# Optimization experiments

Measured on AMD Instinct MI355X. Metric: run time of the kernel, lower is better.

## Reference

```python
import jax, jax.numpy as jnp
import numpy as np

H = 8          # num_attention_heads
E = 768        # hidden_size
D = E // H     # attention_head_size = 96
LN_EPS = 1e-5


def setup_inputs() -> dict:
    key = jax.random.key(0)
    ks = jax.random.split(key, 12)
    B, S = 2, 2048
    inp = {
        "hidden_states": jax.random.normal(ks[0], (B, S, E), jnp.float32),
        "distance_matrix": jax.random.uniform(ks[1], (B, S, S), jnp.float32),
        "angle_matrix": jax.random.uniform(ks[2], (B, S, S), jnp.float32),
        "attention_mask": jnp.ones((B, S), jnp.float32),
        # Linear params, stored [in, out] so y = x @ W + b
        "Wq": jax.random.normal(ks[3], (E, E), jnp.float32) * 0.02,
        "bq": jnp.zeros((E,), jnp.float32),
        "Wk": jax.random.normal(ks[4], (E, E), jnp.float32) * 0.02,
        "bk": jnp.zeros((E,), jnp.float32),
        "Wv": jax.random.normal(ks[5], (E, E), jnp.float32) * 0.02,
        "bv": jnp.zeros((E,), jnp.float32),
        # distance_embedding / angle_embedding: Linear(1,1) -> scalar w,b
        "dist_w": jax.random.normal(ks[6], (), jnp.float32) * 0.5,
        "dist_b": jnp.zeros((), jnp.float32),
        "ang_w": jax.random.normal(ks[7], (), jnp.float32) * 0.5,
        "ang_b": jnp.zeros((), jnp.float32),
        "Wo": jax.random.normal(ks[8], (E, E), jnp.float32) * 0.02,
        "bo": jnp.zeros((E,), jnp.float32),
        "ln_gamma": jnp.ones((E,), jnp.float32),
        "ln_beta": jnp.zeros((E,), jnp.float32),
    }
    return inp


def _attention(hidden_states, distance_matrix, angle_matrix, attention_mask,
               Wq, bq, Wk, bk, Wv, bv, dist_w, dist_b, ang_w, ang_b,
               Wo, bo, ln_gamma, ln_beta):
    B, S, _ = hidden_states.shape
    # project and split heads -> [B, H, S, D]
    def heads(x):
        return x.reshape(B, S, H, D).transpose(0, 2, 1, 3)
    q = heads(hidden_states @ Wq + bq)
    k = heads(hidden_states @ Wk + bk)
    v = heads(hidden_states @ Wv + bv)

    scores = jnp.einsum("bhqd,bhkd->bhqk", q, k) / jnp.sqrt(jnp.float32(D))
    # fused pairwise biases, broadcast over heads
    bias = (dist_w * distance_matrix + dist_b) + (ang_w * angle_matrix + ang_b)
    scores = scores + bias[:, None, :, :]
    # additive mask: mask is [B, S] over key dim
    scores = scores + ((1.0 - attention_mask) * -10000.0)[:, None, None, :]

    probs = jax.nn.softmax(scores, axis=-1)  # dropout is identity at eval
    ctx = jnp.einsum("bhqk,bhkd->bhqd", probs, v)
    ctx = ctx.transpose(0, 2, 1, 3).reshape(B, S, E)

    out = ctx @ Wo + bo  # output dropout identity at eval
    res = out + hidden_states
    mu = jnp.mean(res, axis=-1, keepdims=True)
    var = jnp.var(res, axis=-1, keepdims=True)
    out = (res - mu) * jax.lax.rsqrt(var + LN_EPS) * ln_gamma + ln_beta
    return out, probs


def reference(hidden_states, distance_matrix, angle_matrix, attention_mask,
              Wq, bq, Wk, bk, Wv, bv, dist_w, dist_b, ang_w, ang_b,
              Wo, bo, ln_gamma, ln_beta):
    return _attention(hidden_states, distance_matrix, angle_matrix, attention_mask,
                      Wq, bq, Wk, bk, Wv, bv, dist_w, dist_b, ang_w, ang_b,
                      Wo, bo, ln_gamma, ln_beta)
```

## Files before the change

kernel.cpp:

```cpp
#include <hip/hip_runtime.h>
#include <math.h>

#define S_LEN 2048
#define BATCH 2
#define EMB 768
#define NH 8
#define HD 96
#define NTOK (BATCH*S_LEN)
#define RSQRT_D 0.10206207261596575f

typedef unsigned short u16;
typedef __attribute__((ext_vector_type(8))) short bf16x8;
typedef __attribute__((ext_vector_type(4))) float f32x4;

#define MFMA16(a,b,c) __builtin_amdgcn_mfma_f32_16x16x32_bf16(a,b,c,0,0,0)

__device__ __forceinline__ u16 f2bf(float f){
    unsigned u = __float_as_uint(f);
    return (u16)((u + 0x7fffu + ((u>>16)&1u)) >> 16);
}
__device__ __forceinline__ float bf2f(unsigned u){
    return __uint_as_float(u << 16);
}

union U16x8 { u16 u[8]; float4 f4; };
union U16x4 { u16 u[4]; uint2 v2; };

__global__ __launch_bounds__(256) void cvt_bf16_kernel(
    const float* __restrict__ src, u16* __restrict__ dst, int n4)
{
    int i = blockIdx.x * 256 + threadIdx.x;
    if (i < n4) {
        float4 v = ((const float4*)src)[i];
        U16x4 o;
        o.u[0] = f2bf(v.x); o.u[1] = f2bf(v.y); o.u[2] = f2bf(v.z); o.u[3] = f2bf(v.w);
        *(uint2*)(dst + (size_t)i*4) = o.v2;
    }
}

__global__ __launch_bounds__(256) void transcvt_kernel(
    const float* __restrict__ W, u16* __restrict__ Wt)
{
    __shared__ float T[64][65];
    const int t = threadIdx.x;
    const int k0 = blockIdx.y * 64, n0 = blockIdx.x * 64;
    #pragma unroll
    for (int i = 0; i < 4; ++i) {
        int idx = t + 256*i;
        int r = idx >> 4, c4 = idx & 15;
        float4 v = *(const float4*)(W + (size_t)(k0 + r)*EMB + n0 + c4*4);
        T[r][c4*4+0] = v.x; T[r][c4*4+1] = v.y; T[r][c4*4+2] = v.z; T[r][c4*4+3] = v.w;
    }
    __syncthreads();
    #pragma unroll
    for (int i = 0; i < 2; ++i) {
        int idx = t + 256*i;
        int n = idx >> 3, c = idx & 7;
        U16x8 o;
        #pragma unroll
        for (int e = 0; e < 8; ++e) o.u[e] = f2bf(T[c*8+e][n]);
        *(float4*)(Wt + (size_t)(n0 + n)*EMB + k0 + c*8) = o.f4;
    }
}

__global__ __launch_bounds__(256) void qkv_mfma_kernel(
    const u16* __restrict__ hsb,
    const u16* __restrict__ WqT, const float* __restrict__ bq,
    const u16* __restrict__ WkT, const float* __restrict__ bk,
    const u16* __restrict__ WvT, const float* __restrict__ bv,
    u16* __restrict__ qo, u16* __restrict__ ko, u16* __restrict__ vo)
{
    const u16* Wt; const float* bias; u16* out;
    if (blockIdx.z == 0)      { Wt = WqT; bias = bq; out = qo; }
    else if (blockIdx.z == 1) { Wt = WkT; bias = bk; out = ko; }
    else                      { Wt = WvT; bias = bv; out = vo; }

    __shared__ __align__(16) u16 As[64*64];
    __shared__ __align__(16) u16 Bs[64*64];
    const int tid = threadIdx.x;
    const int w = tid >> 6, lane = tid & 63, lh = lane & 15, g = lane >> 4;
    const int wm = w >> 1, wn = w & 1;
    const int row0 = blockIdx.y * 64, col0 = blockIdx.x * 64;

    f32x4 acc[2][2];
    #pragma unroll
    for (int i = 0; i < 2; ++i)
        #pragma unroll
        for (int j = 0; j < 2; ++j) acc[i][j] = (f32x4){0.f,0.f,0.f,0.f};

    for (int k0 = 0; k0 < EMB; k0 += 64) {
        __syncthreads();
        #pragma unroll
        for (int i = 0; i < 2; ++i) {
            int idx = tid + 256*i;
            int r = idx >> 3, c = idx & 7;
            float4 a4 = *(const float4*)(hsb + (size_t)(row0 + r)*EMB + k0 + c*8);
            *(float4*)(As + ((size_t)r*8 + (c ^ (r & 7)))*8) = a4;
            float4 b4 = *(const float4*)(Wt + (size_t)(col0 + r)*EMB + k0 + c*8);
            *(float4*)(Bs + ((size_t)r*8 + (c ^ (r & 7)))*8) = b4;
        }
        __syncthreads();
        bf16x8 af[2][2], bfr[2][2];
        #pragma unroll
        for (int mt = 0; mt < 2; ++mt)
            #pragma unroll
            for (int kk = 0; kk < 2; ++kk) {
                int r = wm*32 + mt*16 + lh;
                af[mt][kk] = *(const bf16x8*)(As + ((size_t)r*8 + ((kk*4+g) ^ (lh & 7)))*8);
            }
        #pragma unroll
        for (int nt = 0; nt < 2; ++nt)
            #pragma unroll
            for (int kk = 0; kk < 2; ++kk) {
                int r = wn*32 + nt*16 + lh;
                bfr[nt][kk] = *(const bf16x8*)(Bs + ((size_t)r*8 + ((kk*4+g) ^ (lh & 7)))*8);
            }
        #pragma unroll
        for (int mt = 0; mt < 2; ++mt)
            #pragma unroll
            for (int nt = 0; nt < 2; ++nt)
                #pragma unroll
                for (int kk = 0; kk < 2; ++kk)
                    acc[mt][nt] = MFMA16(af[mt][kk], bfr[nt][kk], acc[mt][nt]);
    }

    #pragma unroll
    for (int mt = 0; mt < 2; ++mt)
        #pragma unroll
        for (int nt = 0; nt < 2; ++nt)
            #pragma unroll
            for (int r = 0; r < 4; ++r) {
                int tt = row0 + wm*32 + mt*16 + g*4 + r;
                int o  = col0 + wn*32 + nt*16 + lh;
                float val = acc[mt][nt][r] + bias[o];
                int b = tt >> 11, s = tt & (S_LEN - 1);
                int h = o / HD, d = o - h*HD;
                out[((size_t)(b*NH + h)*S_LEN + s)*HD + d] = f2bf(val);
            }
}

__global__ __launch_bounds__(256) void vtrans_kernel(
    const u16* __restrict__ vb, u16* __restrict__ vt)
{
    const int bh = blockIdx.y;
    const int s0 = blockIdx.x * 64;
    __shared__ __align__(16) u16 T[64*96];
    const int t = threadIdx.x;
    #pragma unroll
    for (int i = 0; i < 3; ++i) {
        int idx = t + 256*i;
        int s = idx / 12, c = idx % 12;
        float4 v = *(const float4*)(vb + ((size_t)bh*S_LEN + s0 + s)*HD + c*8);
        *(float4*)(T + ((size_t)s*12 + c)*8) = v;
    }
    __syncthreads();
    #pragma unroll
    for (int i = 0; i < 3; ++i) {
        int idx = t + 256*i;
        int d = idx >> 3, c = idx & 7;
        U16x8 o;
        #pragma unroll
        for (int e = 0; e < 8; ++e) o.u[e] = T[(size_t)(c*8+e)*HD + d];
        *(float4*)(vt + ((size_t)bh*HD + d)*S_LEN + s0 + c*8) = o.f4;
    }
}

__global__ __launch_bounds__(512) void fused_attn_kernel(
    const u16* __restrict__ qbf, const u16* __restrict__ kbf,
    const u16* __restrict__ vt,
    const float* __restrict__ dist, const float* __restrict__ ang,
    const float* __restrict__ mask,
    const float* __restrict__ pdw, const float* __restrict__ pdb,
    const float* __restrict__ paw, const float* __restrict__ pab,
    float* __restrict__ probs, u16* __restrict__ ctxb)
{
    const int bh = blockIdx.y, b = bh >> 3, h = bh & 7;
    const int q0 = blockIdx.x * 32;
    const int tid = threadIdx.x;
    const int lane = tid & 63, w = tid >> 6, lh = lane & 15, g = lane >> 4;
    const int rt = w >> 2;
    const int ct = w & 3;

    __shared__ __align__(16) u16 Us[32*2048];
    __shared__ __align__(16) u16 Ks[64*96];
    __shared__ __align__(16) float Sf[32*68];
    __shared__ float mL[32];

    const int kr_s = tid / 12, kc_s = tid - (tid / 12) * 12;
    const int kr2_s = (tid + 512) / 12, kc2_s = (tid + 512) - ((tid + 512) / 12) * 12;
    const int vr_s = tid >> 3, vc_s = tid & 7;
    const int vr2_s = (tid + 512) >> 3, vc2_s = (tid + 512) & 7;

    u16* Qtmp = (u16*)Sf;
    if (tid < 384) {
        int r = tid / 12, c = tid % 12;
        float4 v = *(const float4*)(qbf + ((size_t)bh*S_LEN + q0 + r)*HD + c*8);
        *(float4*)(Qtmp + ((size_t)r*12 + (c ^ ((r >> 1) & 3)))*8) = v;
    }
    {
        float4 v = *(const float4*)(kbf + ((size_t)bh*S_LEN + kr_s)*HD + kc_s*8);
        *(float4*)(Ks + ((size_t)kr_s*12 + (kc_s ^ ((kr_s >> 1) & 3)))*8) = v;
        if (tid < 256) {
            float4 v2 = *(const float4*)(kbf + ((size_t)bh*S_LEN + kr2_s)*HD + kc2_s*8);
            *(float4*)(Ks + ((size_t)kr2_s*12 + (kc2_s ^ ((kr2_s >> 1) & 3)))*8) = v2;
        }
    }
    __syncthreads();
    bf16x8 qf[3];
    #pragma unroll
    for (int kk = 0; kk < 3; ++kk) {
        int r = rt*16 + lh;
        qf[kk] = *(const bf16x8*)(Qtmp + ((size_t)r*12 + ((kk*4+g) ^ ((r >> 1) & 3)))*8);
    }
    __syncthreads();

    const float DW = *pdw, AW = *paw, CB = *pdb + *pab;
    const int trow = tid >> 4;
    const int c4   = tid & 15;
    const size_t drow = ((size_t)b*S_LEN + q0 + trow)*S_LEN;
    const int uoff = (trow*8 + ((c4 >> 1) ^ (trow & 7)))*8 + (c4 & 1)*4;

    float lpart = 0.f;

    for (int kt = 0; kt < 32; ++kt) {
        int coff = kt*64 + c4*4;
        float4 kreg0, kreg1;
        if (kt < 31) {
            kreg0 = *(const float4*)(kbf + ((size_t)bh*S_LEN + (kt+1)*64 + kr_s)*HD + kc_s*8);
            if (tid < 256)
                kreg1 = *(const float4*)(kbf + ((size_t)bh*S_LEN + (kt+1)*64 + kr2_s)*HD + kc2_s*8);
        }
        float4 d4 = *(const float4*)(dist + drow + coff);
        float4 g4 = *(const float4*)(ang  + drow + coff);
        float4 m4 = *(const float4*)(mask + b*S_LEN + coff);

        f32x4 acc = (f32x4){0.f,0.f,0.f,0.f};
        #pragma unroll
        for (int kk = 0; kk < 3; ++kk) {
            int kr = ct*16 + lh;
            bf16x8 kf = *(const bf16x8*)(Ks + ((size_t)kr*12 + ((kk*4+g) ^ ((kr >> 1) & 3)))*8);
            acc = MFMA16(qf[kk], kf, acc);
        }
        #pragma unroll
        for (int r = 0; r < 4; ++r)
            Sf[(rt*16 + g*4 + r)*68 + ct*16 + lh] = acc[r];
        __syncthreads();

        float4 s4 = *(const float4*)&Sf[trow*68 + c4*4];
        float e0 = __expf(s4.x*RSQRT_D + DW*d4.x + AW*g4.x + CB + (1.f - m4.x) * -10000.f);
        float e1 = __expf(s4.y*RSQRT_D + DW*d4.y + AW*g4.y + CB + (1.f - m4.y) * -10000.f);
        float e2 = __expf(s4.z*RSQRT_D + DW*d4.z + AW*g4.z + CB + (1.f - m4.z) * -10000.f);
        float e3 = __expf(s4.w*RSQRT_D + DW*d4.w + AW*g4.w + CB + (1.f - m4.w) * -10000.f);
        lpart += (e0 + e1) + (e2 + e3);
        U16x4 uk;
        uk.u[0] = f2bf(e0); uk.u[1] = f2bf(e1); uk.u[2] = f2bf(e2); uk.u[3] = f2bf(e3);
        *(uint2*)(Us + (size_t)kt*2048 + uoff) = uk.v2;

        if (kt < 31) {
            *(float4*)(Ks + ((size_t)kr_s*12 + (kc_s ^ ((kr_s >> 1) & 3)))*8) = kreg0;
            if (tid < 256)
                *(float4*)(Ks + ((size_t)kr2_s*12 + (kc2_s ^ ((kr2_s >> 1) & 3)))*8) = kreg1;
        }
        __syncthreads();
    }

    #pragma unroll
    for (int off = 1; off <= 8; off <<= 1) lpart += __shfl_xor(lpart, off);
    if (c4 == 0) mL[trow] = 1.0f / lpart;
    {
        float4 v4 = *(const float4*)(vt + ((size_t)bh*HD + vr_s)*S_LEN + vc_s*8);
        *(float4*)(Ks + ((size_t)vr_s*8 + (vc_s ^ (vr_s & 7)))*8) = v4;
        if (tid < 256) {
            float4 v42 = *(const float4*)(vt + ((size_t)bh*HD + vr2_s)*S_LEN + vc2_s*8);
            *(float4*)(Ks + ((size_t)vr2_s*8 + (vc2_s ^ (vr2_s & 7)))*8) = v42;
        }
    }
    __syncthreads();

    const float invl_row = mL[trow];
    const int dt1 = ct;
    const bool two = (ct < 2);
    const int dt2 = ct + 4;
    f32x4 accA = (f32x4){0.f,0.f,0.f,0.f};
    f32x4 accB = (f32x4){0.f,0.f,0.f,0.f};

    for (int kt = 0; kt < 32; ++kt) {
        float4 vreg0, vreg1;
        if (kt < 31) {
            vreg0 = *(const float4*)(vt + ((size_t)bh*HD + vr_s)*S_LEN + (kt+1)*64 + vc_s*8);
            if (tid < 256)
                vreg1 = *(const float4*)(vt + ((size_t)bh*HD + vr2_s)*S_LEN + (kt+1)*64 + vc2_s*8);
        }
        {
            uint2 uu = *(const uint2*)(Us + (size_t)kt*2048 + uoff);
            float4 p;
            p.x = bf2f(uu.x & 0xffffu)*invl_row; p.y = bf2f(uu.x >> 16)*invl_row;
            p.z = bf2f(uu.y & 0xffffu)*invl_row; p.w = bf2f(uu.y >> 16)*invl_row;
            *(float4*)(probs + ((size_t)bh*S_LEN + q0 + trow)*S_LEN + kt*64 + c4*4) = p;
        }
        int prow = rt*16 + lh;
        bf16x8 pa[2];
        #pragma unroll
        for (int kk = 0; kk < 2; ++kk)
            pa[kk] = *(const bf16x8*)(Us + (size_t)kt*2048 + ((size_t)prow*8 + ((kk*4+g) ^ (prow & 7)))*8);
        #pragma unroll
        for (int kk = 0; kk < 2; ++kk) {
            int vr = dt1*16 + lh;
            bf16x8 vf = *(const bf16x8*)(Ks + ((size_t)vr*8 + ((kk*4+g) ^ (vr & 7)))*8);
            accA = MFMA16(pa[kk], vf, accA);
        }
        if (two) {
            #pragma unroll
            for (int kk = 0; kk < 2; ++kk) {
                int vr = dt2*16 + lh;
                bf16x8 vf = *(const bf16x8*)(Ks + ((size_t)vr*8 + ((kk*4+g) ^ (vr & 7)))*8);
                accB = MFMA16(pa[kk], vf, accB);
            }
        }
        __syncthreads();
        if (kt < 31) {
            *(float4*)(Ks + ((size_t)vr_s*8 + (vc_s ^ (vr_s & 7)))*8) = vreg0;
            if (tid < 256)
                *(float4*)(Ks + ((size_t)vr2_s*8 + (vc2_s ^ (vr2_s & 7)))*8) = vreg1;
        }
        __syncthreads();
    }

    float ils[4];
    #pragma unroll
    for (int r = 0; r < 4; ++r) ils[r] = mL[rt*16 + g*4 + r];
    #pragma unroll
    for (int r = 0; r < 4; ++r) {
        int qrow = q0 + rt*16 + g*4 + r;
        ctxb[((size_t)(b*S_LEN + qrow))*EMB + h*HD + dt1*16 + lh] = f2bf(accA[r] * ils[r]);
        if (two)
            ctxb[((size_t)(b*S_LEN + qrow))*EMB + h*HD + dt2*16 + lh] = f2bf(accB[r] * ils[r]);
    }
}

__global__ __launch_bounds__(256) void out_mfma_kernel(
    const u16* __restrict__ ctxb, const u16* __restrict__ WoT,
    const float* __restrict__ bo, const float* __restrict__ hs,
    float* __restrict__ res)
{
    __shared__ __align__(16) u16 As[64*64];
    __shared__ __align__(16) u16 Bs[64*64];
    const int tid = threadIdx.x;
    const int w = tid >> 6, lane = tid & 63, lh = lane & 15, g = lane >> 4;
    const int wm = w >> 1, wn = w & 1;
    const int row0 = blockIdx.y * 64, col0 = blockIdx.x * 64;

    f32x4 acc[2][2];
    #pragma unroll
    for (int i = 0; i < 2; ++i)
        #pragma unroll
        for (int j = 0; j < 2; ++j) acc[i][j] = (f32x4){0.f,0.f,0.f,0.f};

    for (int k0 = 0; k0 < EMB; k0 += 64) {
        __syncthreads();
        #pragma unroll
        for (int i = 0; i < 2; ++i) {
            int idx = tid + 256*i;
            int r = idx >> 3, c = idx & 7;
            float4 a4 = *(const float4*)(ctxb + (size_t)(row0 + r)*EMB + k0 + c*8);
            *(float4*)(As + ((size_t)r*8 + (c ^ (r & 7)))*8) = a4;
            float4 b4 = *(const float4*)(WoT + (size_t)(col0 + r)*EMB + k0 + c*8);
            *(float4*)(Bs + ((size_t)r*8 + (c ^ (r & 7)))*8) = b4;
        }
        __syncthreads();
        bf16x8 af[2][2], bfr[2][2];
        #pragma unroll
        for (int mt = 0; mt < 2; ++mt)
            #pragma unroll
            for (int kk = 0; kk < 2; ++kk) {
                int r = wm*32 + mt*16 + lh;
                af[mt][kk] = *(const bf16x8*)(As + ((size_t)r*8 + ((kk*4+g) ^ (lh & 7)))*8);
            }
        #pragma unroll
        for (int nt = 0; nt < 2; ++nt)
            #pragma unroll
            for (int kk = 0; kk < 2; ++kk) {
                int r = wn*32 + nt*16 + lh;
                bfr[nt][kk] = *(const bf16x8*)(Bs + ((size_t)r*8 + ((kk*4+g) ^ (lh & 7)))*8);
            }
        #pragma unroll
        for (int mt = 0; mt < 2; ++mt)
            #pragma unroll
            for (int nt = 0; nt < 2; ++nt)
                #pragma unroll
                for (int kk = 0; kk < 2; ++kk)
                    acc[mt][nt] = MFMA16(af[mt][kk], bfr[nt][kk], acc[mt][nt]);
    }

    #pragma unroll
    for (int mt = 0; mt < 2; ++mt)
        #pragma unroll
        for (int nt = 0; nt < 2; ++nt)
            #pragma unroll
            for (int r = 0; r < 4; ++r) {
                int tt = row0 + wm*32 + mt*16 + g*4 + r;
                int o  = col0 + wn*32 + nt*16 + lh;
                res[(size_t)tt*EMB + o] = acc[mt][nt][r] + bo[o] + hs[(size_t)tt*EMB + o];
            }
}

__device__ __forceinline__ float block_sum256(float v, float* red) {
    #pragma unroll
    for (int off = 32; off > 0; off >>= 1) v += __shfl_down(v, off);
    int lane = threadIdx.x & 63, w = threadIdx.x >> 6;
    __syncthreads();
    if (lane == 0) red[w] = v;
    __syncthreads();
    return red[0] + red[1] + red[2] + red[3];
}

__global__ __launch_bounds__(256) void ln_kernel(
    float* __restrict__ res, const float* __restrict__ gamma, const float* __restrict__ beta)
{
    const int t = blockIdx.x;
    float* row = res + (size_t)t * EMB;
    const int tid = threadIdx.x;
    __shared__ float red[4];

    float x0 = row[tid], x1 = row[tid + 256], x2 = row[tid + 512];
    float s = block_sum256(x0 + x1 + x2, red);
    float mu = s * (1.0f / (float)EMB);
    float d0 = x0 - mu, d1 = x1 - mu, d2 = x2 - mu;
    float sq = block_sum256(d0*d0 + d1*d1 + d2*d2, red);
    float var = sq * (1.0f / (float)EMB);
    float scale = rsqrtf(var + 1e-5f);

    row[tid]       = d0 * scale * gamma[tid]       + beta[tid];
    row[tid + 256] = d1 * scale * gamma[tid + 256] + beta[tid + 256];
    row[tid + 512] = d2 * scale * gamma[tid + 512] + beta[tid + 512];
}

extern "C" void kernel_launch(void* const* d_in, const int* in_sizes, int n_in,
                              void* d_out, int out_size, void* d_ws, size_t ws_size,
                              hipStream_t stream)
{
    (void)in_sizes; (void)n_in; (void)out_size; (void)ws_size;

    const float* hs   = (const float*)d_in[0];
    const float* dist = (const float*)d_in[1];
    const float* ang  = (const float*)d_in[2];
    const float* mask = (const float*)d_in[3];
    const float* Wq = (const float*)d_in[4];  const float* bq = (const float*)d_in[5];
    const float* Wk = (const float*)d_in[6];  const float* bk = (const float*)d_in[7];
    const float* Wv = (const float*)d_in[8];  const float* bv = (const float*)d_in[9];
    const float* dw = (const float*)d_in[10]; const float* db = (const float*)d_in[11];
    const float* aw = (const float*)d_in[12]; const float* ab = (const float*)d_in[13];
    const float* Wo = (const float*)d_in[14]; const float* bo = (const float*)d_in[15];
    const float* gamma = (const float*)d_in[16]; const float* beta = (const float*)d_in[17];

    float* out   = (float*)d_out;
    float* probs = out + (size_t)NTOK * EMB;

    u16* hsb = (u16*)d_ws;
    u16* WqT = hsb + (size_t)NTOK*EMB;
    u16* WkT = WqT + (size_t)EMB*EMB;
    u16* WvT = WkT + (size_t)EMB*EMB;
    u16* WoT = WvT + (size_t)EMB*EMB;
    u16* qb  = WoT + (size_t)EMB*EMB;
    u16* kb  = qb + (size_t)NTOK*EMB;
    u16* vb  = kb + (size_t)NTOK*EMB;
    u16* vtb = vb + (size_t)NTOK*EMB;
    u16* ctxb = qb;

    cvt_bf16_kernel<<<dim3(NTOK*EMB/4/256), dim3(256), 0, stream>>>(hs, hsb, NTOK*EMB/4);
    transcvt_kernel<<<dim3(12,12), dim3(256), 0, stream>>>(Wq, WqT);
    transcvt_kernel<<<dim3(12,12), dim3(256), 0, stream>>>(Wk, WkT);
    transcvt_kernel<<<dim3(12,12), dim3(256), 0, stream>>>(Wv, WvT);
    transcvt_kernel<<<dim3(12,12), dim3(256), 0, stream>>>(Wo, WoT);

    qkv_mfma_kernel<<<dim3(EMB/64, NTOK/64, 3), dim3(256), 0, stream>>>(
        hsb, WqT, bq, WkT, bk, WvT, bv, qb, kb, vb);

    vtrans_kernel<<<dim3(S_LEN/64, BATCH*NH), dim3(256), 0, stream>>>(vb, vtb);

    fused_attn_kernel<<<dim3(S_LEN/32, BATCH*NH), dim3(512), 0, stream>>>(
        qb, kb, vtb, dist, ang, mask, dw, db, aw, ab, probs, ctxb);

    out_mfma_kernel<<<dim3(EMB/64, NTOK/64), dim3(256), 0, stream>>>(
        ctxb, WoT, bo, hs, out);

    ln_kernel<<<dim3(NTOK), dim3(256), 0, stream>>>(out, gamma, beta);
}
```

Baseline: 267.3 us.

## Double-buffer K/V tiles and use per-warp score scratch to halve block barriers

```diff
diff --git a/kernel.cpp b/kernel.cpp
--- a/kernel.cpp
+++ b/kernel.cpp
@@ -182,16 +182,18 @@
     const int ct = w & 3;
 
     __shared__ __align__(16) u16 Us[32*2048];
-    __shared__ __align__(16) u16 Ks[64*96];
-    __shared__ __align__(16) float Sf[32*68];
-    __shared__ float mL[32];
-
-    const int kr_s = tid / 12, kc_s = tid - (tid / 12) * 12;
-    const int kr2_s = (tid + 512) / 12, kc2_s = (tid + 512) - ((tid + 512) / 12) * 12;
+    __shared__ __align__(16) u16 KV[2*64*96];
+    __shared__ __align__(16) float Sfw[8*256];
+
+    u16* Ks0 = KV;
+    u16* Ks1 = KV + 6144;
+
+    const int kr_s = tid / 12, kc_s = tid - (tid/12)*12;
+    const int kr2_s = (tid+512)/12, kc2_s = (tid+512) - ((tid+512)/12)*12;
     const int vr_s = tid >> 3, vc_s = tid & 7;
-    const int vr2_s = (tid + 512) >> 3, vc2_s = (tid + 512) & 7;
-
-    u16* Qtmp = (u16*)Sf;
+    const int vr2_s = (tid+512) >> 3, vc2_s = (tid+512) & 7;
+
+    u16* Qtmp = (u16*)Sfw;
     if (tid < 384) {
         int r = tid / 12, c = tid % 12;
         float4 v = *(const float4*)(qbf + ((size_t)bh*S_LEN + q0 + r)*HD + c*8);
@@ -199,10 +201,10 @@
     }
     {
         float4 v = *(const float4*)(kbf + ((size_t)bh*S_LEN + kr_s)*HD + kc_s*8);
-        *(float4*)(Ks + ((size_t)kr_s*12 + (kc_s ^ ((kr_s >> 1) & 3)))*8) = v;
+        *(float4*)(Ks0 + ((size_t)kr_s*12 + (kc_s ^ ((kr_s >> 1) & 3)))*8) = v;
         if (tid < 256) {
             float4 v2 = *(const float4*)(kbf + ((size_t)bh*S_LEN + kr2_s)*HD + kc2_s*8);
-            *(float4*)(Ks + ((size_t)kr2_s*12 + (kc2_s ^ ((kr2_s >> 1) & 3)))*8) = v2;
+            *(float4*)(Ks0 + ((size_t)kr2_s*12 + (kc2_s ^ ((kr2_s >> 1) & 3)))*8) = v2;
         }
     }
     __syncthreads();
@@ -215,38 +217,42 @@
     __syncthreads();
 
     const float DW = *pdw, AW = *paw, CB = *pdb + *pab;
-    const int trow = tid >> 4;
-    const int c4   = tid & 15;
-    const size_t drow = ((size_t)b*S_LEN + q0 + trow)*S_LEN;
-    const int uoff = (trow*8 + ((c4 >> 1) ^ (trow & 7)))*8 + (c4 & 1)*4;
+
+    const int prow = lane >> 2;
+    const int pc   = lane & 3;
+    const int erow = rt*16 + prow;
+    const size_t drowbase = ((size_t)b*S_LEN + q0 + erow)*S_LEN;
+    const int ecol = ct*16 + pc*4;
+    const int uoffA = (erow*8 + ((ct*2 + (pc>>1)) ^ (erow & 7)))*8 + (pc & 1)*4;
+    float* Sfme = Sfw + w*256;
 
     float lpart = 0.f;
 
     for (int kt = 0; kt < 32; ++kt) {
-        int coff = kt*64 + c4*4;
+        const u16* Kcur = (kt & 1) ? Ks1 : Ks0;
+        u16*       Knxt = (kt & 1) ? Ks0 : Ks1;
         float4 kreg0, kreg1;
         if (kt < 31) {
             kreg0 = *(const float4*)(kbf + ((size_t)bh*S_LEN + (kt+1)*64 + kr_s)*HD + kc_s*8);
             if (tid < 256)
                 kreg1 = *(const float4*)(kbf + ((size_t)bh*S_LEN + (kt+1)*64 + kr2_s)*HD + kc2_s*8);
         }
-        float4 d4 = *(const float4*)(dist + drow + coff);
-        float4 g4 = *(const float4*)(ang  + drow + coff);
-        float4 m4 = *(const float4*)(mask + b*S_LEN + coff);
+        float4 d4 = *(const float4*)(dist + drowbase + kt*64 + ecol);
+        float4 g4 = *(const float4*)(ang  + drowbase + kt*64 + ecol);
+        float4 m4 = *(const float4*)(mask + b*S_LEN + kt*64 + ecol);
 
         f32x4 acc = (f32x4){0.f,0.f,0.f,0.f};
         #pragma unroll
         for (int kk = 0; kk < 3; ++kk) {
             int kr = ct*16 + lh;
-            bf16x8 kf = *(const bf16x8*)(Ks + ((size_t)kr*12 + ((kk*4+g) ^ ((kr >> 1) & 3)))*8);
+            bf16x8 kf = *(const bf16x8*)(Kcur + ((size_t)kr*12 + ((kk*4+g) ^ ((kr >> 1) & 3)))*8);
             acc = MFMA16(qf[kk], kf, acc);
         }
         #pragma unroll
         for (int r = 0; r < 4; ++r)
-            Sf[(rt*16 + g*4 + r)*68 + ct*16 + lh] = acc[r];
-        __syncthreads();
-
-        float4 s4 = *(const float4*)&Sf[trow*68 + c4*4];
+            Sfme[(g*4 + r)*16 + lh] = acc[r];
+        float4 s4 = *(const float4*)&Sfme[prow*16 + pc*4];
+
         float e0 = __expf(s4.x*RSQRT_D + DW*d4.x + AW*g4.x + CB + (1.f - m4.x) * -10000.f);
         float e1 = __expf(s4.y*RSQRT_D + DW*d4.y + AW*g4.y + CB + (1.f - m4.y) * -10000.f);
         float e2 = __expf(s4.z*RSQRT_D + DW*d4.z + AW*g4.z + CB + (1.f - m4.z) * -10000.f);
@@ -254,30 +260,50 @@
         lpart += (e0 + e1) + (e2 + e3);
         U16x4 uk;
         uk.u[0] = f2bf(e0); uk.u[1] = f2bf(e1); uk.u[2] = f2bf(e2); uk.u[3] = f2bf(e3);
-        *(uint2*)(Us + (size_t)kt*2048 + uoff) = uk.v2;
+        *(uint2*)(Us + (size_t)kt*2048 + uoffA) = uk.v2;
 
         if (kt < 31) {
-            *(float4*)(Ks + ((size_t)kr_s*12 + (kc_s ^ ((kr_s >> 1) & 3)))*8) = kreg0;
+            *(float4*)(Knxt + ((size_t)kr_s*12 + (kc_s ^ ((kr_s >> 1) & 3)))*8) = kreg0;
             if (tid < 256)
-                *(float4*)(Ks + ((size_t)kr2_s*12 + (kc2_s ^ ((kr2_s >> 1) & 3)))*8) = kreg1;
+                *(float4*)(Knxt + ((size_t)kr2_s*12 + (kc2_s ^ ((kr2_s >> 1) & 3)))*8) = kreg1;
         }
         __syncthreads();
     }
 
-    #pragma unroll
-    for (int off = 1; off <= 8; off <<= 1) lpart += __shfl_xor(lpart, off);
-    if (c4 == 0) mL[trow] = 1.0f / lpart;
+    lpart += __shfl_xor(lpart, 1);
+    lpart += __shfl_xor(lpart, 2);
+    float* mLp = (float*)KV;
+    if (pc == 0) mLp[w*16 + prow] = lpart;
+    __syncthreads();
+
+    const int trowB = tid >> 4;
+    const int c4B   = tid & 15;
+    float invl_row = 1.0f / (mLp[((trowB>>4)*4 + 0)*16 + (trowB & 15)]
+                           + mLp[((trowB>>4)*4 + 1)*16 + (trowB & 15)]
+                           + mLp[((trowB>>4)*4 + 2)*16 + (trowB & 15)]
+                           + mLp[((trowB>>4)*4 + 3)*16 + (trowB & 15)]);
+    float ils[4];
+    #pragma unroll
+    for (int r = 0; r < 4; ++r) {
+        int rr = g*4 + r;
+        ils[r] = 1.0f / (mLp[(rt*4 + 0)*16 + rr] + mLp[(rt*4 + 1)*16 + rr]
+                       + mLp[(rt*4 + 2)*16 + rr] + mLp[(rt*4 + 3)*16 + rr]);
+    }
+    __syncthreads();
+
+    u16* Vs0 = KV;
+    u16* Vs1 = KV + 6144;
     {
         float4 v4 = *(const float4*)(vt + ((size_t)bh*HD + vr_s)*S_LEN + vc_s*8);
-        *(float4*)(Ks + ((size_t)vr_s*8 + (vc_s ^ (vr_s & 7)))*8) = v4;
+        *(float4*)(Vs0 + ((size_t)vr_s*8 + (vc_s ^ (vr_s & 7)))*8) = v4;
         if (tid < 256) {
             float4 v42 = *(const float4*)(vt + ((size_t)bh*HD + vr2_s)*S_LEN + vc2_s*8);
-            *(float4*)(Ks + ((size_t)vr2_s*8 + (vc2_s ^ (vr2_s & 7)))*8) = v42;
-        }
-    }
-    __syncthreads();
-
-    const float invl_row = mL[trow];
+            *(float4*)(Vs0 + ((size_t)vr2_s*8 + (vc2_s ^ (vr2_s & 7)))*8) = v42;
+        }
+    }
+    __syncthreads();
+
+    const int uoffB = (trowB*8 + ((c4B >> 1) ^ (trowB & 7)))*8 + (c4B & 1)*4;
     const int dt1 = ct;
     const bool two = (ct < 2);
     const int dt2 = ct + 4;
@@ -285,6 +311,8 @@
     f32x4 accB = (f32x4){0.f,0.f,0.f,0.f};
 
     for (int kt = 0; kt < 32; ++kt) {
+        const u16* Vcur = (kt & 1) ? Vs1 : Vs0;
+        u16*       Vnxt = (kt & 1) ? Vs0 : Vs1;
         float4 vreg0, vreg1;
         if (kt < 31) {
             vreg0 = *(const float4*)(vt + ((size_t)bh*HD + vr_s)*S_LEN + (kt+1)*64 + vc_s*8);
@@ -292,43 +320,39 @@
                 vreg1 = *(const float4*)(vt + ((size_t)bh*HD + vr2_s)*S_LEN + (kt+1)*64 + vc2_s*8);
         }
         {
-            uint2 uu = *(const uint2*)(Us + (size_t)kt*2048 + uoff);
+            uint2 uu = *(const uint2*)(Us + (size_t)kt*2048 + uoffB);
             float4 p;
             p.x = bf2f(uu.x & 0xffffu)*invl_row; p.y = bf2f(uu.x >> 16)*invl_row;
             p.z = bf2f(uu.y & 0xffffu)*invl_row; p.w = bf2f(uu.y >> 16)*invl_row;
-            *(float4*)(probs + ((size_t)bh*S_LEN + q0 + trow)*S_LEN + kt*64 + c4*4) = p;
-        }
-        int prow = rt*16 + lh;
+            *(float4*)(probs + ((size_t)bh*S_LEN + q0 + trowB)*S_LEN + kt*64 + c4B*4) = p;
+        }
+        int prowB = rt*16 + lh;
         bf16x8 pa[2];
         #pragma unroll
         for (int kk = 0; kk < 2; ++kk)
-            pa[kk] = *(const bf16x8*)(Us + (size_t)kt*2048 + ((size_t)prow*8 + ((kk*4+g) ^ (prow & 7)))*8);
+            pa[kk] = *(const bf16x8*)(Us + (size_t)kt*2048 + ((size_t)prowB*8 + ((kk*4+g) ^ (prowB & 7)))*8);
         #pragma unroll
         for (int kk = 0; kk < 2; ++kk) {
             int vr = dt1*16 + lh;
-            bf16x8 vf = *(const bf16x8*)(Ks + ((size_t)vr*8 + ((kk*4+g) ^ (vr & 7)))*8);
+            bf16x8 vf = *(const bf16x8*)(Vcur + ((size_t)vr*8 + ((kk*4+g) ^ (vr & 7)))*8);
             accA = MFMA16(pa[kk], vf, accA);
         }
         if (two) {
             #pragma unroll
             for (int kk = 0; kk < 2; ++kk) {
                 int vr = dt2*16 + lh;
-                bf16x8 vf = *(const bf16x8*)(Ks + ((size_t)vr*8 + ((kk*4+g) ^ (vr & 7)))*8);
+                bf16x8 vf = *(const bf16x8*)(Vcur + ((size_t)vr*8 + ((kk*4+g) ^ (vr & 7)))*8);
                 accB = MFMA16(pa[kk], vf, accB);
             }
         }
+        if (kt < 31) {
+            *(float4*)(Vnxt + ((size_t)vr_s*8 + (vc_s ^ (vr_s & 7)))*8) = vreg0;
+            if (tid < 256)
+                *(float4*)(Vnxt + ((size_t)vr2_s*8 + (vc2_s ^ (vr2_s & 7)))*8) = vreg1;
+        }
         __syncthreads();
-        if (kt < 31) {
-            *(float4*)(Ks + ((size_t)vr_s*8 + (vc_s ^ (vr_s & 7)))*8) = vreg0;
-            if (tid < 256)
-                *(float4*)(Ks + ((size_t)vr2_s*8 + (vc2_s ^ (vr2_s & 7)))*8) = vreg1;
-        }
-        __syncthreads();
-    }
-
-    float ils[4];
-    #pragma unroll
-    for (int r = 0; r < 4; ++r) ils[r] = mL[rt*16 + g*4 + r];
+    }
+
     #pragma unroll
     for (int r = 0; r < 4; ++r) {
         int qrow = q0 + rt*16 + g*4 + r;
```

After: 275.3 us. 3.0% more time.
